# Kernel tuning notes

Hardware: AMD Instinct MI355X
Metric: run time of the kernel (lower is better)

Reference implementation:

```python
import jax, jax.numpy as jnp
import numpy as np
import math

N = 100000
E = 3200000
D_IN = 512
HID = 512
N_CLASSES = 64


def _uniform_param(key, shape, fan_out):
    std = 1.0 / math.sqrt(fan_out)
    return jax.random.uniform(key, shape, dtype=jnp.float32, minval=-std, maxval=std)


def setup_inputs() -> dict:
    key = jax.random.key(0)
    ks = jax.random.split(key, 12)
    X = jax.random.normal(ks[0], (N, D_IN), dtype=jnp.float32)
    edge_src = jax.random.randint(ks[1], (E,), 0, N, dtype=jnp.int32)
    edge_dst = jax.random.randint(ks[2], (E,), 0, N, dtype=jnp.int32)
    edge_w = jax.random.uniform(ks[3], (E,), dtype=jnp.float32)
    # layer sizes: [D_IN] + hidden_layers + [N_CLASSES]
    W0 = _uniform_param(ks[4], (D_IN, HID), HID)
    b0 = _uniform_param(ks[5], (HID,), HID)
    W1 = _uniform_param(ks[6], (HID, HID), HID)
    b1 = _uniform_param(ks[7], (HID,), HID)
    W2 = _uniform_param(ks[8], (HID, N_CLASSES), N_CLASSES)
    b2 = _uniform_param(ks[9], (N_CLASSES,), N_CLASSES)
    return {
        "X": X, "edge_src": edge_src, "edge_dst": edge_dst, "edge_w": edge_w,
        "W0": W0, "b0": b0, "W1": W1, "b1": b1, "W2": W2, "b2": b2,
    }


def _spmm(edge_src, edge_dst, edge_w, H):
    # out[i] = sum_{edges (i<-j)} w * H[j]; rows = edge_dst, cols = edge_src
    msgs = edge_w[:, None] * H[edge_src]          # [E, K]
    return jax.ops.segment_sum(msgs, edge_dst, num_segments=N)


def _gcn_layer(edge_src, edge_dst, edge_w, H, W, b):
    H = H @ W                                      # [N, out]
    H = _spmm(edge_src, edge_dst, edge_w, H)
    return H + b


def reference(X, edge_src, edge_dst, edge_w, W0, b0, W1, b1, W2, b2):
    # inference mode: dropout is identity (training=False)
    H = _gcn_layer(edge_src, edge_dst, edge_w, X, W0, b0)
    H = jax.nn.relu(H)
    H = _gcn_layer(edge_src, edge_dst, edge_w, H, W1, b1)
    H = jax.nn.relu(H)
    H = _gcn_layer(edge_src, edge_dst, edge_w, H, W2, b2)
    return jax.nn.softmax(H, axis=-1)              # [N, C]
```

## Files before the change

### kernel.cpp

```cpp
#include <hip/hip_runtime.h>
#include <hip/hip_bf16.h>
#include <cstdint>
#include <cstddef>

#define GN 100000
#define GE 3200000

typedef __attribute__((ext_vector_type(8))) _Float16 f16x8;
typedef __attribute__((ext_vector_type(4))) _Float16 f16x4;
typedef __attribute__((ext_vector_type(4))) float f32x4;


__global__ void k_zero(int* __restrict__ p, int n) {
    int i = blockIdx.x * blockDim.x + threadIdx.x;
    if (i < n) p[i] = 0;
}

__global__ void k_hist(const int* __restrict__ dst, int* __restrict__ cnt, int e) {
    for (int i = blockIdx.x * blockDim.x + threadIdx.x; i < e; i += gridDim.x * blockDim.x)
        atomicAdd(&cnt[dst[i]], 1);
}

__global__ void k_chunksum(const int* __restrict__ cnt, int* __restrict__ bsum, int n) {
    __shared__ int s[256];
    int b = blockIdx.x, t = threadIdx.x;
    int i0 = b * 512;
    int v = 0;
    int i1 = i0 + t;        if (i1 < n) v += cnt[i1];
    int i2 = i0 + 256 + t;  if (i2 < n) v += cnt[i2];
    s[t] = v; __syncthreads();
    for (int d = 128; d > 0; d >>= 1) {
        if (t < d) s[t] += s[t + d];
        __syncthreads();
    }
    if (t == 0) bsum[b] = s[0];
}

__global__ void k_scanb(const int* __restrict__ bsum, int* __restrict__ boff, int nb,
                        int* __restrict__ row_ptr, int n) {
    if (threadIdx.x == 0 && blockIdx.x == 0) {
        int acc = 0;
        for (int b = 0; b < nb; b++) { boff[b] = acc; acc += bsum[b]; }
        row_ptr[n] = acc;
    }
}

__global__ void k_scanw(const int* __restrict__ cnt, const int* __restrict__ boff,
                        int* __restrict__ row_ptr, int* __restrict__ cursor, int n) {
    __shared__ int s[512];
    int b = blockIdx.x, t = threadIdx.x;
    int i = b * 512 + t;
    int x = (i < n) ? cnt[i] : 0;
    s[t] = x; __syncthreads();
    for (int d = 1; d < 512; d <<= 1) {
        int v = (t >= d) ? s[t - d] : 0;
        __syncthreads();
        s[t] += v;
        __syncthreads();
    }
    int excl = s[t] - x + boff[b];
    if (i < n) { row_ptr[i] = excl; cursor[i] = excl; }
}

__global__ void k_scatter(const int* __restrict__ src, const int* __restrict__ dst,
                          const float* __restrict__ w, int* __restrict__ cursor,
                          int* __restrict__ ecol, float* __restrict__ ew, int e) {
    for (int i = blockIdx.x * blockDim.x + threadIdx.x; i < e; i += gridDim.x * blockDim.x) {
        int d = dst[i];
        int p = atomicAdd(&cursor[d], 1);
        ecol[p] = src[i];
        ew[p]   = w[i];
    }
}


__global__ void k_transp_split(const float* __restrict__ W,
                               _Float16* __restrict__ Wth, _Float16* __restrict__ Wtl,
                               int K, int M) {
    __shared__ float tile[32][33];
    int bx = blockIdx.x * 32;
    int by = blockIdx.y * 32;
    int tx = threadIdx.x, ty = threadIdx.y;
    for (int i = ty; i < 32; i += 8)
        tile[i][tx] = W[(size_t)(by + i) * M + bx + tx];
    __syncthreads();
    for (int i = ty; i < 32; i += 8) {
        float w = tile[tx][i];
        _Float16 h = (_Float16)w;
        _Float16 l = (_Float16)(w - (float)h);
        Wth[(size_t)(bx + i) * K + by + tx] = h;
        Wtl[(size_t)(bx + i) * K + by + tx] = l;
    }
}


template<int BN, typename OutT>
__global__ __launch_bounds__(256, 2) void k_gemm_split(const float* __restrict__ A,
                                                       const _Float16* __restrict__ Bth,
                                                       const _Float16* __restrict__ Btl,
                                                       OutT* __restrict__ C,
                                                       int n, int m) {
    constexpr int NI  = BN / 32;
    constexpr int BIT = BN / 32;
    __shared__ _Float16 Ash[128 * 64];
    __shared__ _Float16 Asl[128 * 64];
    __shared__ _Float16 Bsh[BN * 64];
    __shared__ _Float16 Bsl[BN * 64];
    int tid = threadIdx.x;
    int wv = tid >> 6, lane = tid & 63;
    int wr = wv >> 1, wc = wv & 1;
    int r0 = blockIdx.y * 128;
    int c0 = blockIdx.x * BN;

    float4 areg[8];
    f16x8 bregh[BIT], bregl[BIT];
    f32x4 acc[4][NI];
    #pragma unroll
    for (int i = 0; i < 4; i++)
        #pragma unroll
        for (int j = 0; j < NI; j++)
            acc[i][j] = (f32x4){0.f, 0.f, 0.f, 0.f};

    auto aload = [&](int kt) {
        #pragma unroll
        for (int i = 0; i < 8; ++i) {
            int q = tid + 256 * i;
            int row = q >> 4, c4 = q & 15;
            int gr = r0 + row; if (gr >= n) gr = n - 1;
            areg[i] = *(const float4*)(A + (size_t)gr * 512 + kt * 64 + c4 * 4);
        }
        #pragma unroll
        for (int i = 0; i < BIT; ++i) {
            int q = tid + 256 * i;
            int col = q >> 3, c = q & 7;
            size_t off = (size_t)(c0 + col) * 512 + kt * 64 + c * 8;
            bregh[i] = *(const f16x8*)(Bth + off);
            bregl[i] = *(const f16x8*)(Btl + off);
        }
    };

    aload(0);
    for (int kt = 0; kt < 8; ++kt) {
        __syncthreads();
        #pragma unroll
        for (int i = 0; i < 8; ++i) {
            int q = tid + 256 * i;
            int row = q >> 4, c4 = q & 15;
            int g = c4 ^ ((row & 7) << 1);
            float4 a = areg[i];
            _Float16 hx = (_Float16)a.x, hy = (_Float16)a.y;
            _Float16 hz = (_Float16)a.z, hw = (_Float16)a.w;
            f16x4 h = { hx, hy, hz, hw };
            f16x4 l = { (_Float16)(a.x - (float)hx), (_Float16)(a.y - (float)hy),
                        (_Float16)(a.z - (float)hz), (_Float16)(a.w - (float)hw) };
            *(f16x4*)&Ash[row * 64 + g * 4] = h;
            *(f16x4*)&Asl[row * 64 + g * 4] = l;
        }
        #pragma unroll
        for (int i = 0; i < BIT; ++i) {
            int q = tid + 256 * i;
            int col = q >> 3, c = q & 7;
            int idx = col * 64 + ((c ^ (col & 7)) * 8);
            *(f16x8*)&Bsh[idx] = bregh[i];
            *(f16x8*)&Bsl[idx] = bregl[i];
        }
        __syncthreads();
        if (kt < 7) aload(kt + 1);
        #pragma unroll
        for (int ks = 0; ks < 2; ++ks) {
            f16x8 afh[4], afl[4], bfh[NI], bfl[NI];
            int cch = ks * 4 + (lane >> 4);
            #pragma unroll
            for (int mi = 0; mi < 4; ++mi) {
                int row = wr * 64 + mi * 16 + (lane & 15);
                int idx = row * 64 + (((cch * 2) ^ ((row & 7) << 1)) * 4);
                afh[mi] = *(const f16x8*)&Ash[idx];
                afl[mi] = *(const f16x8*)&Asl[idx];
            }
            #pragma unroll
            for (int ni = 0; ni < NI; ++ni) {
                int col = wc * (BN / 2) + ni * 16 + (lane & 15);
                int idx = col * 64 + ((cch ^ (col & 7)) * 8);
                bfh[ni] = *(const f16x8*)&Bsh[idx];
                bfl[ni] = *(const f16x8*)&Bsl[idx];
            }
            #pragma unroll
            for (int mi = 0; mi < 4; ++mi)
                #pragma unroll
                for (int ni = 0; ni < NI; ++ni) {
                    acc[mi][ni] = __builtin_amdgcn_mfma_f32_16x16x32_f16(
                        afh[mi], bfl[ni], acc[mi][ni], 0, 0, 0);
                    acc[mi][ni] = __builtin_amdgcn_mfma_f32_16x16x32_f16(
                        afl[mi], bfh[ni], acc[mi][ni], 0, 0, 0);
                    acc[mi][ni] = __builtin_amdgcn_mfma_f32_16x16x32_f16(
                        afh[mi], bfh[ni], acc[mi][ni], 0, 0, 0);
                }
        }
    }

    #pragma unroll
    for (int mi = 0; mi < 4; ++mi) {
        #pragma unroll
        for (int j = 0; j < 4; ++j) {
            int gr = r0 + wr * 64 + mi * 16 + (lane >> 4) * 4 + j;
            if (gr < n) {
                #pragma unroll
                for (int ni = 0; ni < NI; ++ni) {
                    int gc = c0 + wc * (BN / 2) + ni * 16 + (lane & 15);
                    C[(size_t)gr * m + gc] = (OutT)acc[mi][ni][j];
                }
            }
        }
    }
}


template<int BN, typename OutT>
__global__ __launch_bounds__(256, 2) void k_gemm_f16w2(const _Float16* __restrict__ A,
                                                       const _Float16* __restrict__ Bth,
                                                       const _Float16* __restrict__ Btl,
                                                       OutT* __restrict__ C,
                                                       int n, int m) {
    constexpr int NI  = BN / 32;
    constexpr int BIT = BN / 32;
    __shared__ _Float16 As[128 * 64];
    __shared__ _Float16 Bsh[BN * 64];
    __shared__ _Float16 Bsl[BN * 64];
    int tid = threadIdx.x;
    int wv = tid >> 6, lane = tid & 63;
    int wr = wv >> 1, wc = wv & 1;
    int r0 = blockIdx.y * 128;
    int c0 = blockIdx.x * BN;

    f16x8 areg[4], bregh[BIT], bregl[BIT];
    f32x4 acc[4][NI];
    #pragma unroll
    for (int i = 0; i < 4; i++)
        #pragma unroll
        for (int j = 0; j < NI; j++)
            acc[i][j] = (f32x4){0.f, 0.f, 0.f, 0.f};

    auto aload = [&](int kt) {
        #pragma unroll
        for (int i = 0; i < 4; ++i) {
            int q = tid + 256 * i;
            int row = q >> 3, c = q & 7;
            int gr = r0 + row; if (gr >= n) gr = n - 1;
            areg[i] = *(const f16x8*)(A + (size_t)gr * 512 + kt * 64 + c * 8);
        }
        #pragma unroll
        for (int i = 0; i < BIT; ++i) {
            int q = tid + 256 * i;
            int col = q >> 3, c = q & 7;
            size_t off = (size_t)(c0 + col) * 512 + kt * 64 + c * 8;
            bregh[i] = *(const f16x8*)(Bth + off);
            bregl[i] = *(const f16x8*)(Btl + off);
        }
    };

    aload(0);
    for (int kt = 0; kt < 8; ++kt) {
        __syncthreads();
        #pragma unroll
        for (int i = 0; i < 4; ++i) {
            int q = tid + 256 * i;
            int row = q >> 3, c = q & 7;
            *(f16x8*)&As[row * 64 + ((c ^ (row & 7)) * 8)] = areg[i];
        }
        #pragma unroll
        for (int i = 0; i < BIT; ++i) {
            int q = tid + 256 * i;
            int col = q >> 3, c = q & 7;
            int idx = col * 64 + ((c ^ (col & 7)) * 8);
            *(f16x8*)&Bsh[idx] = bregh[i];
            *(f16x8*)&Bsl[idx] = bregl[i];
        }
        __syncthreads();
        if (kt < 7) aload(kt + 1);
        #pragma unroll
        for (int ks = 0; ks < 2; ++ks) {
            f16x8 af[4], bfh[NI], bfl[NI];
            int cch = ks * 4 + (lane >> 4);
            #pragma unroll
            for (int mi = 0; mi < 4; ++mi) {
                int row = wr * 64 + mi * 16 + (lane & 15);
                af[mi] = *(const f16x8*)&As[row * 64 + ((cch ^ (row & 7)) * 8)];
            }
            #pragma unroll
            for (int ni = 0; ni < NI; ++ni) {
                int col = wc * (BN / 2) + ni * 16 + (lane & 15);
                int idx = col * 64 + ((cch ^ (col & 7)) * 8);
                bfh[ni] = *(const f16x8*)&Bsh[idx];
                bfl[ni] = *(const f16x8*)&Bsl[idx];
            }
            #pragma unroll
            for (int mi = 0; mi < 4; ++mi)
                #pragma unroll
                for (int ni = 0; ni < NI; ++ni) {
                    acc[mi][ni] = __builtin_amdgcn_mfma_f32_16x16x32_f16(
                        af[mi], bfl[ni], acc[mi][ni], 0, 0, 0);
                    acc[mi][ni] = __builtin_amdgcn_mfma_f32_16x16x32_f16(
                        af[mi], bfh[ni], acc[mi][ni], 0, 0, 0);
                }
        }
    }

    #pragma unroll
    for (int mi = 0; mi < 4; ++mi) {
        #pragma unroll
        for (int j = 0; j < 4; ++j) {
            int gr = r0 + wr * 64 + mi * 16 + (lane >> 4) * 4 + j;
            if (gr < n) {
                #pragma unroll
                for (int ni = 0; ni < NI; ++ni) {
                    int gc = c0 + wc * (BN / 2) + ni * 16 + (lane & 15);
                    C[(size_t)gr * m + gc] = (OutT)acc[mi][ni][j];
                }
            }
        }
    }
}


__global__ __launch_bounds__(64) void k_spmm512_h2h(const int* __restrict__ rowp,
                                                    const int* __restrict__ ecol,
                                                    const float* __restrict__ ew,
                                                    const _Float16* __restrict__ H,
                                                    const float* __restrict__ bias,
                                                    _Float16* __restrict__ out,
                                                    int relu) {
    int row = blockIdx.x;
    int t = threadIdx.x;
    int s0 = rowp[row], s1 = rowp[row + 1];
    const f16x8* H8 = (const f16x8*)H;
    float a0 = 0.f, a1 = 0.f, a2 = 0.f, a3 = 0.f;
    float a4 = 0.f, a5 = 0.f, a6 = 0.f, a7 = 0.f;
    __shared__ int   lc[64];
    __shared__ float lw[64];
    for (int base = s0; base < s1; base += 64) {
        int nn = s1 - base; if (nn > 64) nn = 64;
        __syncthreads();
        if (t < nn) {
            lc[t] = __builtin_nontemporal_load(ecol + base + t);
            lw[t] = __builtin_nontemporal_load(ew + base + t);
        }
        __syncthreads();
        int e = 0;
        for (; e + 8 <= nn; e += 8) {
            f16x8 h0 = H8[(size_t)lc[e]     * 64 + t];
            f16x8 h1 = H8[(size_t)lc[e + 1] * 64 + t];
            f16x8 h2 = H8[(size_t)lc[e + 2] * 64 + t];
            f16x8 h3 = H8[(size_t)lc[e + 3] * 64 + t];
            f16x8 h4 = H8[(size_t)lc[e + 4] * 64 + t];
            f16x8 h5 = H8[(size_t)lc[e + 5] * 64 + t];
            f16x8 h6 = H8[(size_t)lc[e + 6] * 64 + t];
            f16x8 h7 = H8[(size_t)lc[e + 7] * 64 + t];
            float w0 = lw[e],     w1 = lw[e + 1], w2 = lw[e + 2], w3 = lw[e + 3];
            float w4 = lw[e + 4], w5 = lw[e + 5], w6 = lw[e + 6], w7 = lw[e + 7];
            a0 += w0*(float)h0[0] + w1*(float)h1[0] + w2*(float)h2[0] + w3*(float)h3[0]
                + w4*(float)h4[0] + w5*(float)h5[0] + w6*(float)h6[0] + w7*(float)h7[0];
            a1 += w0*(float)h0[1] + w1*(float)h1[1] + w2*(float)h2[1] + w3*(float)h3[1]
                + w4*(float)h4[1] + w5*(float)h5[1] + w6*(float)h6[1] + w7*(float)h7[1];
            a2 += w0*(float)h0[2] + w1*(float)h1[2] + w2*(float)h2[2] + w3*(float)h3[2]
                + w4*(float)h4[2] + w5*(float)h5[2] + w6*(float)h6[2] + w7*(float)h7[2];
            a3 += w0*(float)h0[3] + w1*(float)h1[3] + w2*(float)h2[3] + w3*(float)h3[3]
                + w4*(float)h4[3] + w5*(float)h5[3] + w6*(float)h6[3] + w7*(float)h7[3];
            a4 += w0*(float)h0[4] + w1*(float)h1[4] + w2*(float)h2[4] + w3*(float)h3[4]
                + w4*(float)h4[4] + w5*(float)h5[4] + w6*(float)h6[4] + w7*(float)h7[4];
            a5 += w0*(float)h0[5] + w1*(float)h1[5] + w2*(float)h2[5] + w3*(float)h3[5]
                + w4*(float)h4[5] + w5*(float)h5[5] + w6*(float)h6[5] + w7*(float)h7[5];
            a6 += w0*(float)h0[6] + w1*(float)h1[6] + w2*(float)h2[6] + w3*(float)h3[6]
                + w4*(float)h4[6] + w5*(float)h5[6] + w6*(float)h6[6] + w7*(float)h7[6];
            a7 += w0*(float)h0[7] + w1*(float)h1[7] + w2*(float)h2[7] + w3*(float)h3[7]
                + w4*(float)h4[7] + w5*(float)h5[7] + w6*(float)h6[7] + w7*(float)h7[7];
        }
        for (; e < nn; ++e) {
            f16x8 h = H8[(size_t)lc[e] * 64 + t]; float w = lw[e];
            a0 += w * (float)h[0]; a1 += w * (float)h[1];
            a2 += w * (float)h[2]; a3 += w * (float)h[3];
            a4 += w * (float)h[4]; a5 += w * (float)h[5];
            a6 += w * (float)h[6]; a7 += w * (float)h[7];
        }
    }
    const float4* b4 = (const float4*)bias;
    float4 blo = b4[t * 2], bhi = b4[t * 2 + 1];
    a0 += blo.x; a1 += blo.y; a2 += blo.z; a3 += blo.w;
    a4 += bhi.x; a5 += bhi.y; a6 += bhi.z; a7 += bhi.w;
    if (relu) {
        a0 = fmaxf(a0, 0.f); a1 = fmaxf(a1, 0.f); a2 = fmaxf(a2, 0.f); a3 = fmaxf(a3, 0.f);
        a4 = fmaxf(a4, 0.f); a5 = fmaxf(a5, 0.f); a6 = fmaxf(a6, 0.f); a7 = fmaxf(a7, 0.f);
    }
    f16x8 o = { (_Float16)a0, (_Float16)a1, (_Float16)a2, (_Float16)a3,
                (_Float16)a4, (_Float16)a5, (_Float16)a6, (_Float16)a7 };
    ((f16x8*)out)[(size_t)row * 64 + t] = o;
}


__global__ __launch_bounds__(256) void k_spmm64_softmax(const int* __restrict__ rowp,
                                                        const int* __restrict__ ecol,
                                                        const float* __restrict__ ew,
                                                        const _Float16* __restrict__ H,
                                                        const float* __restrict__ bias,
                                                        float* __restrict__ out, int n) {
    int wid  = threadIdx.x >> 6;
    int lane = threadIdx.x & 63;
    int row  = blockIdx.x * 4 + wid;
    if (row >= n) return;
    int s0 = rowp[row], s1 = rowp[row + 1];
    float acc = 0.f;
    int e = s0;
    for (; e + 4 <= s1; e += 4) {
        float h0 = (float)H[(size_t)ecol[e]     * 64 + lane];
        float h1 = (float)H[(size_t)ecol[e + 1] * 64 + lane];
        float h2 = (float)H[(size_t)ecol[e + 2] * 64 + lane];
        float h3 = (float)H[(size_t)ecol[e + 3] * 64 + lane];
        acc += ew[e] * h0 + ew[e + 1] * h1 + ew[e + 2] * h2 + ew[e + 3] * h3;
    }
    for (; e < s1; ++e)
        acc += ew[e] * (float)H[(size_t)ecol[e] * 64 + lane];
    acc += bias[lane];
    float m = acc;
    for (int d = 32; d > 0; d >>= 1) m = fmaxf(m, __shfl_xor(m, d));
    float p = __expf(acc - m);
    float s = p;
    for (int d = 32; d > 0; d >>= 1) s += __shfl_xor(s, d);
    __builtin_nontemporal_store(p / s, out + (size_t)row * 64 + lane);
}


extern "C" void kernel_launch(void* const* d_in, const int* in_sizes, int n_in,
                              void* d_out, int out_size, void* d_ws, size_t ws_size,
                              hipStream_t stream) {
    const float* X    = (const float*)d_in[0];
    const int*   esrc = (const int*)d_in[1];
    const int*   edst = (const int*)d_in[2];
    const float* ewin = (const float*)d_in[3];
    const float* W0   = (const float*)d_in[4];
    const float* b0   = (const float*)d_in[5];
    const float* W1   = (const float*)d_in[6];
    const float* b1   = (const float*)d_in[7];
    const float* W2   = (const float*)d_in[8];
    const float* b2   = (const float*)d_in[9];
    float* out = (float*)d_out;

    const int N = GN;
    const int E = GE;

    uint8_t* p = (uint8_t*)d_ws;
    auto alloc = [&](size_t bytes) -> void* {
        void* r = (void*)p;
        p += (bytes + 255) & ~(size_t)255;
        return r;
    };
    _Float16* bufM  = (_Float16*)alloc((size_t)N * 512 * 2);
    _Float16* bufG  = (_Float16*)alloc((size_t)N * 512 * 2);
    _Float16* bufC3 = (_Float16*)alloc((size_t)N * 64 * 2);
    _Float16* W0th  = (_Float16*)alloc((size_t)512 * 512 * 2);
    _Float16* W0tl  = (_Float16*)alloc((size_t)512 * 512 * 2);
    _Float16* W1th  = (_Float16*)alloc((size_t)512 * 512 * 2);
    _Float16* W1tl  = (_Float16*)alloc((size_t)512 * 512 * 2);
    _Float16* W2th  = (_Float16*)alloc((size_t)64 * 512 * 2);
    _Float16* W2tl  = (_Float16*)alloc((size_t)64 * 512 * 2);
    int*   cnt     = (int*)alloc((size_t)N * 4);
    int*   row_ptr = (int*)alloc((size_t)(N + 1) * 4);
    int*   cursor  = (int*)alloc((size_t)N * 4);
    int*   ecol    = (int*)alloc((size_t)E * 4);
    float* ewv     = (float*)alloc((size_t)E * 4);
    int*   bsum    = (int*)alloc(1024 * 4);
    int*   boff    = (int*)alloc(1024 * 4);

    int nch = (N + 511) / 512;
    k_zero<<<(N + 255) / 256, 256, 0, stream>>>(cnt, N);
    k_hist<<<2048, 256, 0, stream>>>(edst, cnt, E);
    k_chunksum<<<nch, 256, 0, stream>>>(cnt, bsum, N);
    k_scanb<<<1, 64, 0, stream>>>(bsum, boff, nch, row_ptr, N);
    k_scanw<<<nch, 512, 0, stream>>>(cnt, boff, row_ptr, cursor, N);
    k_scatter<<<2048, 256, 0, stream>>>(esrc, edst, ewin, cursor, ecol, ewv, E);

    k_transp_split<<<dim3(16, 16), dim3(32, 8), 0, stream>>>(W0, W0th, W0tl, 512, 512);
    k_transp_split<<<dim3(16, 16), dim3(32, 8), 0, stream>>>(W1, W1th, W1tl, 512, 512);
    k_transp_split<<<dim3(2, 16),  dim3(32, 8), 0, stream>>>(W2, W2th, W2tl, 512, 64);

    int gy = (N + 127) / 128;
    k_gemm_split<128, _Float16><<<dim3(4, gy), 256, 0, stream>>>(X, W0th, W0tl, bufM, N, 512);
    k_spmm512_h2h<<<N, 64, 0, stream>>>(row_ptr, ecol, ewv, bufM, b0, bufG, 1);
    k_gemm_f16w2<128, _Float16><<<dim3(4, gy), 256, 0, stream>>>(bufG, W1th, W1tl, bufM, N, 512);
    k_spmm512_h2h<<<N, 64, 0, stream>>>(row_ptr, ecol, ewv, bufM, b1, bufG, 1);
    k_gemm_f16w2<64, _Float16><<<dim3(1, gy), 256, 0, stream>>>(bufG, W2th, W2tl, bufC3, N, 64);
    k_spmm64_softmax<<<(N + 3) / 4, 256, 0, stream>>>(row_ptr, ecol, ewv, bufC3, b2, out, N);
}
```

Baseline: 1.709 ms.

## Split 512-wide SpMM into two column-slice passes and keep layer-3 logits in fp32

The 512-column SpMM now runs as two launches, each gathering one 256-column half of the neighbour rows with 8-byte loads instead of 16-byte loads. This halves the working set of the random gather per pass so more of it can stay in L2/MALL. The cost is reading the CSR indices and weights twice per layer and an extra launch. Separately, the final 64-class GEMM writes fp32 output and the softmax SpMM reads fp32, doubling that buffer's traffic while removing fp16 rounding.

```diff
diff --git a/kernel.cpp b/kernel.cpp
--- a/kernel.cpp
+++ b/kernel.cpp
@@ -322,19 +322,19 @@
 }
 
 
-__global__ __launch_bounds__(64) void k_spmm512_h2h(const int* __restrict__ rowp,
-                                                    const int* __restrict__ ecol,
-                                                    const float* __restrict__ ew,
-                                                    const _Float16* __restrict__ H,
-                                                    const float* __restrict__ bias,
-                                                    _Float16* __restrict__ out,
-                                                    int relu) {
+__global__ __launch_bounds__(64) void k_spmm512_slice(const int* __restrict__ rowp,
+                                                      const int* __restrict__ ecol,
+                                                      const float* __restrict__ ew,
+                                                      const _Float16* __restrict__ H,
+                                                      const float* __restrict__ bias,
+                                                      _Float16* __restrict__ out,
+                                                      int relu, int slice) {
     int row = blockIdx.x;
     int t = threadIdx.x;
     int s0 = rowp[row], s1 = rowp[row + 1];
-    const f16x8* H8 = (const f16x8*)H;
+    const f16x4* H4 = (const f16x4*)H;
+    int vo = slice * 64 + t;
     float a0 = 0.f, a1 = 0.f, a2 = 0.f, a3 = 0.f;
-    float a4 = 0.f, a5 = 0.f, a6 = 0.f, a7 = 0.f;
     __shared__ int   lc[64];
     __shared__ float lw[64];
     for (int base = s0; base < s1; base += 64) {
@@ -347,14 +347,14 @@
         __syncthreads();
         int e = 0;
         for (; e + 8 <= nn; e += 8) {
-            f16x8 h0 = H8[(size_t)lc[e]     * 64 + t];
-            f16x8 h1 = H8[(size_t)lc[e + 1] * 64 + t];
-            f16x8 h2 = H8[(size_t)lc[e + 2] * 64 + t];
-            f16x8 h3 = H8[(size_t)lc[e + 3] * 64 + t];
-            f16x8 h4 = H8[(size_t)lc[e + 4] * 64 + t];
-            f16x8 h5 = H8[(size_t)lc[e + 5] * 64 + t];
-            f16x8 h6 = H8[(size_t)lc[e + 6] * 64 + t];
-            f16x8 h7 = H8[(size_t)lc[e + 7] * 64 + t];
+            f16x4 h0 = H4[(size_t)lc[e]     * 128 + vo];
+            f16x4 h1 = H4[(size_t)lc[e + 1] * 128 + vo];
+            f16x4 h2 = H4[(size_t)lc[e + 2] * 128 + vo];
+            f16x4 h3 = H4[(size_t)lc[e + 3] * 128 + vo];
+            f16x4 h4 = H4[(size_t)lc[e + 4] * 128 + vo];
+            f16x4 h5 = H4[(size_t)lc[e + 5] * 128 + vo];
+            f16x4 h6 = H4[(size_t)lc[e + 6] * 128 + vo];
+            f16x4 h7 = H4[(size_t)lc[e + 7] * 128 + vo];
             float w0 = lw[e],     w1 = lw[e + 1], w2 = lw[e + 2], w3 = lw[e + 3];
             float w4 = lw[e + 4], w5 = lw[e + 5], w6 = lw[e + 6], w7 = lw[e + 7];
             a0 += w0*(float)h0[0] + w1*(float)h1[0] + w2*(float)h2[0] + w3*(float)h3[0]
@@ -365,41 +365,28 @@
                 + w4*(float)h4[2] + w5*(float)h5[2] + w6*(float)h6[2] + w7*(float)h7[2];
             a3 += w0*(float)h0[3] + w1*(float)h1[3] + w2*(float)h2[3] + w3*(float)h3[3]
                 + w4*(float)h4[3] + w5*(float)h5[3] + w6*(float)h6[3] + w7*(float)h7[3];
-            a4 += w0*(float)h0[4] + w1*(float)h1[4] + w2*(float)h2[4] + w3*(float)h3[4]
-                + w4*(float)h4[4] + w5*(float)h5[4] + w6*(float)h6[4] + w7*(float)h7[4];
-            a5 += w0*(float)h0[5] + w1*(float)h1[5] + w2*(float)h2[5] + w3*(float)h3[5]
-                + w4*(float)h4[5] + w5*(float)h5[5] + w6*(float)h6[5] + w7*(float)h7[5];
-            a6 += w0*(float)h0[6] + w1*(float)h1[6] + w2*(float)h2[6] + w3*(float)h3[6]
-                + w4*(float)h4[6] + w5*(float)h5[6] + w6*(float)h6[6] + w7*(float)h7[6];
-            a7 += w0*(float)h0[7] + w1*(float)h1[7] + w2*(float)h2[7] + w3*(float)h3[7]
-                + w4*(float)h4[7] + w5*(float)h5[7] + w6*(float)h6[7] + w7*(float)h7[7];
         }
         for (; e < nn; ++e) {
-            f16x8 h = H8[(size_t)lc[e] * 64 + t]; float w = lw[e];
+            f16x4 h = H4[(size_t)lc[e] * 128 + vo]; float w = lw[e];
             a0 += w * (float)h[0]; a1 += w * (float)h[1];
             a2 += w * (float)h[2]; a3 += w * (float)h[3];
-            a4 += w * (float)h[4]; a5 += w * (float)h[5];
-            a6 += w * (float)h[6]; a7 += w * (float)h[7];
-        }
-    }
-    const float4* b4 = (const float4*)bias;
-    float4 blo = b4[t * 2], bhi = b4[t * 2 + 1];
-    a0 += blo.x; a1 += blo.y; a2 += blo.z; a3 += blo.w;
-    a4 += bhi.x; a5 += bhi.y; a6 += bhi.z; a7 += bhi.w;
+        }
+    }
+    float4 b = ((const float4*)bias)[vo];
+    a0 += b.x; a1 += b.y; a2 += b.z; a3 += b.w;
     if (relu) {
-        a0 = fmaxf(a0, 0.f); a1 = fmaxf(a1, 0.f); a2 = fmaxf(a2, 0.f); a3 = fmaxf(a3, 0.f);
-        a4 = fmaxf(a4, 0.f); a5 = fmaxf(a5, 0.f); a6 = fmaxf(a6, 0.f); a7 = fmaxf(a7, 0.f);
-    }
-    f16x8 o = { (_Float16)a0, (_Float16)a1, (_Float16)a2, (_Float16)a3,
-                (_Float16)a4, (_Float16)a5, (_Float16)a6, (_Float16)a7 };
-    ((f16x8*)out)[(size_t)row * 64 + t] = o;
+        a0 = fmaxf(a0, 0.f); a1 = fmaxf(a1, 0.f);
+        a2 = fmaxf(a2, 0.f); a3 = fmaxf(a3, 0.f);
+    }
+    f16x4 o = { (_Float16)a0, (_Float16)a1, (_Float16)a2, (_Float16)a3 };
+    ((f16x4*)out)[(size_t)row * 128 + vo] = o;
 }
 
 
 __global__ __launch_bounds__(256) void k_spmm64_softmax(const int* __restrict__ rowp,
                                                         const int* __restrict__ ecol,
                                                         const float* __restrict__ ew,
-                                                        const _Float16* __restrict__ H,
+                                                        const float* __restrict__ H,
                                                         const float* __restrict__ bias,
                                                         float* __restrict__ out, int n) {
     int wid  = threadIdx.x >> 6;
@@ -410,14 +397,14 @@
     float acc = 0.f;
     int e = s0;
     for (; e + 4 <= s1; e += 4) {
-        float h0 = (float)H[(size_t)ecol[e]     * 64 + lane];
-        float h1 = (float)H[(size_t)ecol[e + 1] * 64 + lane];
-        float h2 = (float)H[(size_t)ecol[e + 2] * 64 + lane];
-        float h3 = (float)H[(size_t)ecol[e + 3] * 64 + lane];
+        float h0 = H[(size_t)ecol[e]     * 64 + lane];
+        float h1 = H[(size_t)ecol[e + 1] * 64 + lane];
+        float h2 = H[(size_t)ecol[e + 2] * 64 + lane];
+        float h3 = H[(size_t)ecol[e + 3] * 64 + lane];
         acc += ew[e] * h0 + ew[e + 1] * h1 + ew[e + 2] * h2 + ew[e + 3] * h3;
     }
     for (; e < s1; ++e)
-        acc += ew[e] * (float)H[(size_t)ecol[e] * 64 + lane];
+        acc += ew[e] * H[(size_t)ecol[e] * 64 + lane];
     acc += bias[lane];
     float m = acc;
     for (int d = 32; d > 0; d >>= 1) m = fmaxf(m, __shfl_xor(m, d));
@@ -454,7 +441,7 @@
     };
     _Float16* bufM  = (_Float16*)alloc((size_t)N * 512 * 2);
     _Float16* bufG  = (_Float16*)alloc((size_t)N * 512 * 2);
-    _Float16* bufC3 = (_Float16*)alloc((size_t)N * 64 * 2);
+    float*    bufC3 = (float*)alloc((size_t)N * 64 * 4);
     _Float16* W0th  = (_Float16*)alloc((size_t)512 * 512 * 2);
     _Float16* W0tl  = (_Float16*)alloc((size_t)512 * 512 * 2);
     _Float16* W1th  = (_Float16*)alloc((size_t)512 * 512 * 2);
@@ -483,9 +470,11 @@
 
     int gy = (N + 127) / 128;
     k_gemm_split<128, _Float16><<<dim3(4, gy), 256, 0, stream>>>(X, W0th, W0tl, bufM, N, 512);
-    k_spmm512_h2h<<<N, 64, 0, stream>>>(row_ptr, ecol, ewv, bufM, b0, bufG, 1);
+    k_spmm512_slice<<<N, 64, 0, stream>>>(row_ptr, ecol, ewv, bufM, b0, bufG, 1, 0);
+    k_spmm512_slice<<<N, 64, 0, stream>>>(row_ptr, ecol, ewv, bufM, b0, bufG, 1, 1);
     k_gemm_f16w2<128, _Float16><<<dim3(4, gy), 256, 0, stream>>>(bufG, W1th, W1tl, bufM, N, 512);
-    k_spmm512_h2h<<<N, 64, 0, stream>>>(row_ptr, ecol, ewv, bufM, b1, bufG, 1);
-    k_gemm_f16w2<64, _Float16><<<dim3(1, gy), 256, 0, stream>>>(bufG, W2th, W2tl, bufC3, N, 64);
+    k_spmm512_slice<<<N, 64, 0, stream>>>(row_ptr, ecol, ewv, bufM, b1, bufG, 1, 0);
+    k_spmm512_slice<<<N, 64, 0, stream>>>(row_ptr, ecol, ewv, bufM, b1, bufG, 1, 1);
+    k_gemm_f16w2<64, float><<<dim3(1, gy), 256, 0, stream>>>(bufG, W2th, W2tl, bufC3, N, 64);
     k_spmm64_softmax<<<(N + 3) / 4, 256, 0, stream>>>(row_ptr, ecol, ewv, bufC3, b2, out, N);
 }
```

After: 1.668 ms. 2.4% less time.

## Interleave CSR column and weight into packed pairs; fp32 final layer buffer

Applied to the files above, without the earlier changes.

Replaces the separate edge column and weight arrays with one interleaved int2 array, so each SpMM edge fetch is a single 8-byte load instead of two scattered 4-byte loads, and the scatter writes one pair. The final-layer GEMM output is now stored as fp32 instead of fp16, which doubles that buffer's gather traffic in the softmax SpMM but removes the conversion and improves accuracy. The f16w2 GEMM launch bounds are also raised to 3 blocks per SM, which may force register spilling.

```diff
diff --git a/kernel.cpp b/kernel.cpp
--- a/kernel.cpp
+++ b/kernel.cpp
@@ -9,6 +9,7 @@
 typedef __attribute__((ext_vector_type(8))) _Float16 f16x8;
 typedef __attribute__((ext_vector_type(4))) _Float16 f16x4;
 typedef __attribute__((ext_vector_type(4))) float f32x4;
+typedef __attribute__((ext_vector_type(2))) int i32x2;
 
 
 __global__ void k_zero(int* __restrict__ p, int n) {
@@ -64,12 +65,12 @@
 
 __global__ void k_scatter(const int* __restrict__ src, const int* __restrict__ dst,
                           const float* __restrict__ w, int* __restrict__ cursor,
-                          int* __restrict__ ecol, float* __restrict__ ew, int e) {
+                          i32x2* __restrict__ epair, int e) {
     for (int i = blockIdx.x * blockDim.x + threadIdx.x; i < e; i += gridDim.x * blockDim.x) {
         int d = dst[i];
         int p = atomicAdd(&cursor[d], 1);
-        ecol[p] = src[i];
-        ew[p]   = w[i];
+        i32x2 v; v.x = src[i]; v.y = __float_as_int(w[i]);
+        epair[p] = v;
     }
 }
 
@@ -216,7 +217,7 @@
 
 
 template<int BN, typename OutT>
-__global__ __launch_bounds__(256, 2) void k_gemm_f16w2(const _Float16* __restrict__ A,
+__global__ __launch_bounds__(256, 3) void k_gemm_f16w2(const _Float16* __restrict__ A,
                                                        const _Float16* __restrict__ Bth,
                                                        const _Float16* __restrict__ Btl,
                                                        OutT* __restrict__ C,
@@ -323,8 +324,7 @@
 
 
 __global__ __launch_bounds__(64) void k_spmm512_h2h(const int* __restrict__ rowp,
-                                                    const int* __restrict__ ecol,
-                                                    const float* __restrict__ ew,
+                                                    const i32x2* __restrict__ epair,
                                                     const _Float16* __restrict__ H,
                                                     const float* __restrict__ bias,
                                                     _Float16* __restrict__ out,
@@ -335,28 +335,28 @@
     const f16x8* H8 = (const f16x8*)H;
     float a0 = 0.f, a1 = 0.f, a2 = 0.f, a3 = 0.f;
     float a4 = 0.f, a5 = 0.f, a6 = 0.f, a7 = 0.f;
-    __shared__ int   lc[64];
-    __shared__ float lw[64];
+    __shared__ i32x2 le[64];
     for (int base = s0; base < s1; base += 64) {
         int nn = s1 - base; if (nn > 64) nn = 64;
         __syncthreads();
-        if (t < nn) {
-            lc[t] = __builtin_nontemporal_load(ecol + base + t);
-            lw[t] = __builtin_nontemporal_load(ew + base + t);
-        }
+        if (t < nn) le[t] = __builtin_nontemporal_load(epair + base + t);
         __syncthreads();
         int e = 0;
         for (; e + 8 <= nn; e += 8) {
-            f16x8 h0 = H8[(size_t)lc[e]     * 64 + t];
-            f16x8 h1 = H8[(size_t)lc[e + 1] * 64 + t];
-            f16x8 h2 = H8[(size_t)lc[e + 2] * 64 + t];
-            f16x8 h3 = H8[(size_t)lc[e + 3] * 64 + t];
-            f16x8 h4 = H8[(size_t)lc[e + 4] * 64 + t];
-            f16x8 h5 = H8[(size_t)lc[e + 5] * 64 + t];
-            f16x8 h6 = H8[(size_t)lc[e + 6] * 64 + t];
-            f16x8 h7 = H8[(size_t)lc[e + 7] * 64 + t];
-            float w0 = lw[e],     w1 = lw[e + 1], w2 = lw[e + 2], w3 = lw[e + 3];
-            float w4 = lw[e + 4], w5 = lw[e + 5], w6 = lw[e + 6], w7 = lw[e + 7];
+            i32x2 p0 = le[e],     p1 = le[e + 1], p2 = le[e + 2], p3 = le[e + 3];
+            i32x2 p4 = le[e + 4], p5 = le[e + 5], p6 = le[e + 6], p7 = le[e + 7];
+            f16x8 h0 = H8[(size_t)p0.x * 64 + t];
+            f16x8 h1 = H8[(size_t)p1.x * 64 + t];
+            f16x8 h2 = H8[(size_t)p2.x * 64 + t];
+            f16x8 h3 = H8[(size_t)p3.x * 64 + t];
+            f16x8 h4 = H8[(size_t)p4.x * 64 + t];
+            f16x8 h5 = H8[(size_t)p5.x * 64 + t];
+            f16x8 h6 = H8[(size_t)p6.x * 64 + t];
+            f16x8 h7 = H8[(size_t)p7.x * 64 + t];
+            float w0 = __int_as_float(p0.y), w1 = __int_as_float(p1.y);
+            float w2 = __int_as_float(p2.y), w3 = __int_as_float(p3.y);
+            float w4 = __int_as_float(p4.y), w5 = __int_as_float(p5.y);
+            float w6 = __int_as_float(p6.y), w7 = __int_as_float(p7.y);
             a0 += w0*(float)h0[0] + w1*(float)h1[0] + w2*(float)h2[0] + w3*(float)h3[0]
                 + w4*(float)h4[0] + w5*(float)h5[0] + w6*(float)h6[0] + w7*(float)h7[0];
             a1 += w0*(float)h0[1] + w1*(float)h1[1] + w2*(float)h2[1] + w3*(float)h3[1]
@@ -375,7 +375,8 @@
                 + w4*(float)h4[7] + w5*(float)h5[7] + w6*(float)h6[7] + w7*(float)h7[7];
         }
         for (; e < nn; ++e) {
-            f16x8 h = H8[(size_t)lc[e] * 64 + t]; float w = lw[e];
+            i32x2 pe = le[e];
+            f16x8 h = H8[(size_t)pe.x * 64 + t]; float w = __int_as_float(pe.y);
             a0 += w * (float)h[0]; a1 += w * (float)h[1];
             a2 += w * (float)h[2]; a3 += w * (float)h[3];
             a4 += w * (float)h[4]; a5 += w * (float)h[5];
@@ -397,9 +398,8 @@
 
 
 __global__ __launch_bounds__(256) void k_spmm64_softmax(const int* __restrict__ rowp,
-                                                        const int* __restrict__ ecol,
-                                                        const float* __restrict__ ew,
-                                                        const _Float16* __restrict__ H,
+                                                        const i32x2* __restrict__ epair,
+                                                        const float* __restrict__ H,
                                                         const float* __restrict__ bias,
                                                         float* __restrict__ out, int n) {
     int wid  = threadIdx.x >> 6;
@@ -410,14 +410,19 @@
     float acc = 0.f;
     int e = s0;
     for (; e + 4 <= s1; e += 4) {
-        float h0 = (float)H[(size_t)ecol[e]     * 64 + lane];
-        float h1 = (float)H[(size_t)ecol[e + 1] * 64 + lane];
-        float h2 = (float)H[(size_t)ecol[e + 2] * 64 + lane];
-        float h3 = (float)H[(size_t)ecol[e + 3] * 64 + lane];
-        acc += ew[e] * h0 + ew[e + 1] * h1 + ew[e + 2] * h2 + ew[e + 3] * h3;
-    }
-    for (; e < s1; ++e)
-        acc += ew[e] * (float)H[(size_t)ecol[e] * 64 + lane];
+        i32x2 p0 = epair[e],     p1 = epair[e + 1];
+        i32x2 p2 = epair[e + 2], p3 = epair[e + 3];
+        float h0 = H[(size_t)p0.x * 64 + lane];
+        float h1 = H[(size_t)p1.x * 64 + lane];
+        float h2 = H[(size_t)p2.x * 64 + lane];
+        float h3 = H[(size_t)p3.x * 64 + lane];
+        acc += __int_as_float(p0.y) * h0 + __int_as_float(p1.y) * h1
+             + __int_as_float(p2.y) * h2 + __int_as_float(p3.y) * h3;
+    }
+    for (; e < s1; ++e) {
+        i32x2 pe = epair[e];
+        acc += __int_as_float(pe.y) * H[(size_t)pe.x * 64 + lane];
+    }
     acc += bias[lane];
     float m = acc;
     for (int d = 32; d > 0; d >>= 1) m = fmaxf(m, __shfl_xor(m, d));
@@ -454,7 +459,7 @@
     };
     _Float16* bufM  = (_Float16*)alloc((size_t)N * 512 * 2);
     _Float16* bufG  = (_Float16*)alloc((size_t)N * 512 * 2);
-    _Float16* bufC3 = (_Float16*)alloc((size_t)N * 64 * 2);
+    float*    bufC3 = (float*)alloc((size_t)N * 64 * 4);
     _Float16* W0th  = (_Float16*)alloc((size_t)512 * 512 * 2);
     _Float16* W0tl  = (_Float16*)alloc((size_t)512 * 512 * 2);
     _Float16* W1th  = (_Float16*)alloc((size_t)512 * 512 * 2);
@@ -464,8 +469,7 @@
     int*   cnt     = (int*)alloc((size_t)N * 4);
     int*   row_ptr = (int*)alloc((size_t)(N + 1) * 4);
     int*   cursor  = (int*)alloc((size_t)N * 4);
-    int*   ecol    = (int*)alloc((size_t)E * 4);
-    float* ewv     = (float*)alloc((size_t)E * 4);
+    i32x2* epair   = (i32x2*)alloc((size_t)E * 8);
     int*   bsum    = (int*)alloc(1024 * 4);
     int*   boff    = (int*)alloc(1024 * 4);
 
@@ -475,7 +479,7 @@
     k_chunksum<<<nch, 256, 0, stream>>>(cnt, bsum, N);
     k_scanb<<<1, 64, 0, stream>>>(bsum, boff, nch, row_ptr, N);
     k_scanw<<<nch, 512, 0, stream>>>(cnt, boff, row_ptr, cursor, N);
-    k_scatter<<<2048, 256, 0, stream>>>(esrc, edst, ewin, cursor, ecol, ewv, E);
+    k_scatter<<<2048, 256, 0, stream>>>(esrc, edst, ewin, cursor, epair, E);
 
     k_transp_split<<<dim3(16, 16), dim3(32, 8), 0, stream>>>(W0, W0th, W0tl, 512, 512);
     k_transp_split<<<dim3(16, 16), dim3(32, 8), 0, stream>>>(W1, W1th, W1tl, 512, 512);
@@ -483,9 +487,9 @@
 
     int gy = (N + 127) / 128;
     k_gemm_split<128, _Float16><<<dim3(4, gy), 256, 0, stream>>>(X, W0th, W0tl, bufM, N, 512);
-    k_spmm512_h2h<<<N, 64, 0, stream>>>(row_ptr, ecol, ewv, bufM, b0, bufG, 1);
+    k_spmm512_h2h<<<N, 64, 0, stream>>>(row_ptr, epair, bufM, b0, bufG, 1);
     k_gemm_f16w2<128, _Float16><<<dim3(4, gy), 256, 0, stream>>>(bufG, W1th, W1tl, bufM, N, 512);
-    k_spmm512_h2h<<<N, 64, 0, stream>>>(row_ptr, ecol, ewv, bufM, b1, bufG, 1);
-    k_gemm_f16w2<64, _Float16><<<dim3(1, gy), 256, 0, stream>>>(bufG, W2th, W2tl, bufC3, N, 64);
-    k_spmm64_softmax<<<(N + 3) / 4, 256, 0, stream>>>(row_ptr, ecol, ewv, bufC3, b2, out, N);
-}
+    k_spmm512_h2h<<<N, 64, 0, stream>>>(row_ptr, epair, bufM, b1, bufG, 1);
+    k_gemm_f16w2<64, float><<<dim3(1, gy), 256, 0, stream>>>(bufG, W2th, W2tl, bufC3, N, 64);
+    k_spmm64_softmax<<<(N + 3) / 4, 256, 0, stream>>>(row_ptr, epair, bufC3, b2, out, N);
+}
```

New measurement: 1.719 ms. No clear change (+0.6%).
